# Optimization experiments

Measured on AMD Instinct MI355X. Metric: run time of the kernel, lower is better.

The kernel has to match this reference:

```python
import jax, jax.numpy as jnp
import numpy as np

INPUT_DIM, HIDDEN_DIM, OUTPUT_DIM = 64, 256, 32
BATCH, SEQ = 256, 1024
# AutoNCP(256, 32, sparsity_level=0.5): motor=32, command=max(int(0.4*224),1)=89, inter=135
LAYER_HID = [135, 89, 32]
LAYER_IN = [INPUT_DIM, 135, 89]


def setup_inputs() -> dict:
    key = jax.random.key(0)
    ks = iter(jax.random.split(key, 64))
    d = {}
    d["x"] = jax.random.normal(next(ks), (BATCH, SEQ, INPUT_DIM), dtype=jnp.float32)
    for l, (fin, hid) in enumerate(zip(LAYER_IN, LAYER_HID)):
        sp = jax.random.bernoulli(next(ks), 0.5, (hid, fin))
        d[f"mask{l}"] = jnp.concatenate([sp, jnp.ones((hid, hid), dtype=bool)], axis=1)
        scale = 1.0 / np.sqrt(fin + hid)
        for name in ("W1", "W2", "Wa", "Wb"):
            d[f"{name}_{l}"] = jax.random.normal(next(ks), (hid, fin + hid), dtype=jnp.float32) * scale
        for name in ("b1", "b2", "ba", "bb"):
            d[f"{name}_{l}"] = jnp.zeros((hid,), dtype=jnp.float32)
    d["fc_W"] = jax.random.normal(next(ks), (HIDDEN_DIM, HIDDEN_DIM), dtype=jnp.float32) * (1.0 / np.sqrt(HIDDEN_DIM))
    d["fc_b"] = jnp.zeros((HIDDEN_DIM,), dtype=jnp.float32)
    return d


def _cfc_cell(inp, h, mask, W1, b1, W2, b2, Wa, ba, Wb, bb):
    # ncps CfCCell, mode='default', no backbone, ts = 1.0
    x = jnp.concatenate([inp, h], axis=1)
    m = mask.astype(W1.dtype)
    ff1 = jnp.tanh(x @ (W1 * m).T + b1)
    ff2 = jnp.tanh(x @ (W2 * m).T + b2)
    t = jax.nn.sigmoid(x @ Wa.T + ba + x @ Wb.T + bb)  # sigmoid(t_a*ts + t_b), ts=1
    return ff1 * (1.0 - t) + t * ff2


def _forward(x, masks, layer_params, fc_W, fc_b):
    B = x.shape[0]
    init = tuple(jnp.zeros((B, h), dtype=x.dtype) for h in LAYER_HID)

    def step(carry, xt):
        hs = list(carry)
        inp = xt
        for l in range(3):  # inter -> command -> motor (WiredCfCCell)
            hs[l] = _cfc_cell(inp, hs[l], masks[l], *layer_params[l])
            inp = hs[l]
        return tuple(hs), None

    carry, _ = jax.lax.scan(step, init, jnp.swapaxes(x, 0, 1))  # scan over time [T,B,D]
    hn = jnp.concatenate(carry, axis=1)  # [B, HIDDEN_DIM] full state
    return hn @ fc_W.T + fc_b


def reference(x, mask0, mask1, mask2,
              W1_0, b1_0, W2_0, b2_0, Wa_0, ba_0, Wb_0, bb_0,
              W1_1, b1_1, W2_1, b2_1, Wa_1, ba_1, Wb_1, bb_1,
              W1_2, b1_2, W2_2, b2_2, Wa_2, ba_2, Wb_2, bb_2,
              fc_W, fc_b):
    masks = (mask0, mask1, mask2)
    lp = ((W1_0, b1_0, W2_0, b2_0, Wa_0, ba_0, Wb_0, bb_0),
          (W1_1, b1_1, W2_1, b2_1, Wa_1, ba_1, Wb_1, bb_1),
          (W1_2, b1_2, W2_2, b2_2, Wa_2, ba_2, Wb_2, bb_2))
    return _forward(x, masks, lp, fc_W, fc_b)
```

## Files before the change

### kernel.cpp

```cpp
#include <hip/hip_runtime.h>


typedef _Float16 half2v __attribute__((ext_vector_type(2)));
typedef _Float16 half8v __attribute__((ext_vector_type(8)));

#define NBLK   256
#define NTHR   512
#define TSTEPS 1024
#define KPAD   224
#define KHALF  112
#define NKB    14

struct Ptrs {
    const float* x;
    const unsigned int* msk[3];
    const float* W1[3];
    const float* W2[3];
    const float* Wa[3];
    const float* Wb[3];
    const float* b1[3];
    const float* b2[3];
    const float* ba[3];
    const float* bb[3];
    const float* fcW;
    const float* fcb;
};

__device__ __forceinline__ float fexp2(float x) {
#if __has_builtin(__builtin_amdgcn_exp2f)
    return __builtin_amdgcn_exp2f(x);
#else
    return exp2f(x);
#endif
}
__device__ __forceinline__ float frcp(float x) {
#if __has_builtin(__builtin_amdgcn_rcpf)
    return __builtin_amdgcn_rcpf(x);
#else
    return 1.0f / x;
#endif
}
__device__ __forceinline__ float fsig(float x) {
    return frcp(1.0f + fexp2(-1.442695041f * x));
}
__device__ __forceinline__ float ftanh(float x) {
    return 2.0f * frcp(1.0f + fexp2(-2.885390082f * x)) - 1.0f;
}

#if __has_builtin(__builtin_amdgcn_fdot2)
#define FD(a, b, c) __builtin_amdgcn_fdot2((a), (b), (c), false)
#else
__device__ __forceinline__ float fd_fallback(half2v a, half2v b, float c) {
    return c + (float)a[0] * (float)b[0] + (float)a[1] * (float)b[1];
}
#define FD(a, b, c) fd_fallback((a), (b), (c))
#endif

__global__ __launch_bounds__(NTHR)
__attribute__((amdgpu_waves_per_eu(2, 2)))
void cfc_kernel(Ptrs P, float* __restrict__ out) {
    __shared__ __align__(16) _Float16 xc[2][3][KPAD];
    __shared__ __align__(16) float hn[256];

    const int tid  = threadIdx.x;
    const int b    = blockIdx.x;
    const int pair = tid >> 1;
    const int half = tid & 1;

    int L, n;
    if (pair < 135)      { L = 0; n = pair; }
    else if (pair < 224) { L = 1; n = pair - 135; }
    else                 { L = 2; n = pair - 224; }
    const int K    = (L == 0) ? 199 : ((L == 1) ? 224 : 121);
    const int HOFF = (L == 0) ? 0   : ((L == 1) ? 135 : 224);

    {
        int* z = (int*)&xc[0][0][0];
        for (int i = tid; i < 2 * 3 * KPAD / 2; i += NTHR) z[i] = 0;
    }
    __syncthreads();

    const int xlane = tid - 448;
    float xpend = 0.0f;
    if (xlane >= 0) {
        xc[0][0][xlane] = (_Float16)P.x[((size_t)b * TSTEPS + 0) * 64 + xlane];
        xpend           = P.x[((size_t)b * TSTEPS + 1) * 64 + xlane];
    }

    const float* W1p        = P.W1[L];
    const float* W2p        = P.W2[L];
    const float* Wap        = P.Wa[L];
    const float* Wbp        = P.Wb[L];
    const unsigned int* mkp = P.msk[L];
    const int nK   = n * K;
    const int koff = half * KHALF;

    half2v wr1[KHALF / 2], wr2[KHALF / 2], wra[KHALF / 2];
#pragma unroll
    for (int i = 0; i < KHALF / 2; ++i) {
        const int k0 = koff + 2 * i, k1 = koff + 2 * i + 1;
        float u0 = 0.f, u1 = 0.f, v0 = 0.f, v1 = 0.f, a0 = 0.f, a1 = 0.f;
        if (k0 < K) {
            const int idx = nK + k0;
            const float mm = (mkp[idx] != 0u) ? 1.0f : 0.0f;
            u0 = W1p[idx] * mm;
            v0 = W2p[idx] * mm;
            a0 = Wap[idx] + Wbp[idx];
        }
        if (k1 < K) {
            const int idx = nK + k1;
            const float mm = (mkp[idx] != 0u) ? 1.0f : 0.0f;
            u1 = W1p[idx] * mm;
            v1 = W2p[idx] * mm;
            a1 = Wap[idx] + Wbp[idx];
        }
        wr1[i] = half2v{(_Float16)u0, (_Float16)u1};
        wr2[i] = half2v{(_Float16)v0, (_Float16)v1};
        wra[i] = half2v{(_Float16)a0, (_Float16)a1};
    }
    const float bv1 = P.b1[L][n];
    const float bv2 = P.b2[L][n];
    const float bva = P.ba[L][n] + P.bb[L][n];
    __syncthreads();

    for (int tick = 0; tick < TSTEPS + 2; ++tick) {
        if (xlane >= 0) {
            if (tick + 1 < TSTEPS)
                xc[(tick + 1) & 1][0][xlane] = (_Float16)xpend;
            if (tick + 2 < TSTEPS)
                xpend = P.x[((size_t)b * TSTEPS + (tick + 2)) * 64 + xlane];
        }

        const int s = tick - L;
        if (s >= 0 && s < TSTEPS) {
            const _Float16* src = &xc[s & 1][L][koff];
            float ac00 = 0.f, ac01 = 0.f, ac10 = 0.f, ac11 = 0.f, ac20 = 0.f, ac21 = 0.f;
#pragma unroll
            for (int kb = 0; kb < NKB; ++kb) {
                const half8v xv = *(const half8v*)(src + kb * 8);
                const half2v x0 = {xv[0], xv[1]};
                const half2v x1 = {xv[2], xv[3]};
                const half2v x2 = {xv[4], xv[5]};
                const half2v x3 = {xv[6], xv[7]};
                const int k4 = kb * 4;
                ac00 = FD(x0, wr1[k4 + 0], ac00);
                ac10 = FD(x0, wr2[k4 + 0], ac10);
                ac20 = FD(x0, wra[k4 + 0], ac20);
                ac01 = FD(x1, wr1[k4 + 1], ac01);
                ac11 = FD(x1, wr2[k4 + 1], ac11);
                ac21 = FD(x1, wra[k4 + 1], ac21);
                ac00 = FD(x2, wr1[k4 + 2], ac00);
                ac10 = FD(x2, wr2[k4 + 2], ac10);
                ac20 = FD(x2, wra[k4 + 2], ac20);
                ac01 = FD(x3, wr1[k4 + 3], ac01);
                ac11 = FD(x3, wr2[k4 + 3], ac11);
                ac21 = FD(x3, wra[k4 + 3], ac21);
            }
            float s1 = ac00 + ac01;
            float s2 = ac10 + ac11;
            float sa = ac20 + ac21;
            s1 += __shfl_xor(s1, 1, 64);
            s2 += __shfl_xor(s2, 1, 64);
            sa += __shfl_xor(sa, 1, 64);
            const float f1 = ftanh(s1 + bv1);
            const float f2 = ftanh(s2 + bv2);
            const float tg = fsig(sa + bva);
            const float h  = f1 + tg * (f2 - f1);
            const _Float16 hv = (_Float16)h;

            const int pA = s & 1;
            const int pB = (s + 1) & 1;
            if (half == 0) {
                if (L == 0)      xc[pA][1][n] = hv;
                else if (L == 1) xc[pA][2][n] = hv;
                if (s == TSTEPS - 1) hn[HOFF + n] = h;
            } else {
                if (L == 0)      xc[pB][0][64 + n]  = hv;
                else if (L == 1) xc[pB][1][135 + n] = hv;
                else             xc[pB][2][89 + n]  = hv;
            }
        }
        __syncthreads();
    }

    {
        const int o = pair;
        const float4* wr = (const float4*)(P.fcW + (size_t)o * 256 + half * 128);
        const float4* hr = (const float4*)(hn + half * 128);
        float acc = half ? 0.0f : P.fcb[o];
#pragma unroll 8
        for (int d = 0; d < 32; ++d) {
            const float4 a = hr[d];
            const float4 w = wr[d];
            acc += a.x * w.x + a.y * w.y + a.z * w.z + a.w * w.w;
        }
        acc += __shfl_xor(acc, 1, 64);
        if (half == 0) out[(size_t)b * 256 + o] = acc;
    }
}

extern "C" void kernel_launch(void* const* d_in, const int* in_sizes, int n_in,
                              void* d_out, int out_size, void* d_ws, size_t ws_size,
                              hipStream_t stream) {
    (void)in_sizes; (void)n_in; (void)out_size; (void)d_ws; (void)ws_size;
    Ptrs P;
    P.x = (const float*)d_in[0];
    for (int l = 0; l < 3; ++l) {
        const int base = 1 + l * 9;
        P.msk[l] = (const unsigned int*)d_in[base + 0];
        P.W1[l]  = (const float*)d_in[base + 1];
        P.W2[l]  = (const float*)d_in[base + 2];
        P.Wa[l]  = (const float*)d_in[base + 3];
        P.Wb[l]  = (const float*)d_in[base + 4];
        P.b1[l]  = (const float*)d_in[base + 5];
        P.b2[l]  = (const float*)d_in[base + 6];
        P.ba[l]  = (const float*)d_in[base + 7];
        P.bb[l]  = (const float*)d_in[base + 8];
    }
    P.fcW = (const float*)d_in[28];
    P.fcb = (const float*)d_in[29];

    hipLaunchKernelGGL(cfc_kernel, dim3(NBLK), dim3(NTHR), 0, stream,
                       P, (float*)d_out);
}
```

Before: 1.472 ms.

## Precompute layer-0 input projections per time window and split thread roles by layer

Measured after the change: 1.636 ms. 1.11x slower.

```diff
diff --git a/kernel.cpp b/kernel.cpp
--- a/kernel.cpp
+++ b/kernel.cpp
@@ -8,8 +8,7 @@
 #define NTHR   512
 #define TSTEPS 1024
 #define KPAD   224
-#define KHALF  112
-#define NKB    14
+#define WIN    64
 
 struct Ptrs {
     const float* x;
@@ -56,23 +55,64 @@
 #define FD(a, b, c) fd_fallback((a), (b), (c))
 #endif
 
+__device__ __forceinline__ half2v h2(_Float16 a, _Float16 b) { return half2v{a, b}; }
+
+__device__ __forceinline__ float psum(float x) { return x + __shfl_xor(x, 1, 64); }
+
+#define DOJOB(jj_) { \
+    const int jm = (jj_) >> 7, jn = (jj_) & 127; \
+    const float* Wp = (jm == 0) ? P.W1[0] : (jm == 1) ? P.W2[0] : P.Wa[0]; \
+    const float* Wq = P.Wb[0]; \
+    const unsigned int* mk0 = P.msk[0]; \
+    const int base = jn * 199; \
+    half2v wrow[32]; \
+    _Pragma("unroll") \
+    for (int i2 = 0; i2 < 32; ++i2) { \
+        const int k = 2 * i2; \
+        float v0 = Wp[base + k], v1 = Wp[base + k + 1]; \
+        if (jm == 2) { v0 += Wq[base + k]; v1 += Wq[base + k + 1]; } \
+        else { \
+            v0 = (mk0[base + k] != 0u) ? v0 : 0.0f; \
+            v1 = (mk0[base + k + 1] != 0u) ? v1 : 0.0f; \
+        } \
+        wrow[i2] = h2((_Float16)v0, (_Float16)v1); \
+    } \
+    for (int ti = 0; ti < WIN; ++ti) { \
+        float acc = 0.0f; \
+        _Pragma("unroll") \
+        for (int q = 0; q < 8; ++q) { \
+            const half8v xq = *(const half8v*)&xwin[ti][8 * q]; \
+            acc = FD(h2(xq[0], xq[1]), wrow[4 * q + 0], acc); \
+            acc = FD(h2(xq[2], xq[3]), wrow[4 * q + 1], acc); \
+            acc = FD(h2(xq[4], xq[5]), wrow[4 * q + 2], acc); \
+            acc = FD(h2(xq[6], xq[7]), wrow[4 * q + 3], acc); \
+        } \
+        U[jm][ti][jn] = (_Float16)acc; \
+    } \
+}
+
+#define WINDOW_BLOCK(STAGE_, JOBS_) \
+    if ((tick & (WIN - 1)) == 0 && tick < TSTEPS) { \
+        __syncthreads(); \
+        STAGE_ \
+        __syncthreads(); \
+        JOBS_ \
+        __syncthreads(); \
+    }
+
 __global__ __launch_bounds__(NTHR)
-__attribute__((amdgpu_waves_per_eu(2, 2)))
 void cfc_kernel(Ptrs P, float* __restrict__ out) {
     __shared__ __align__(16) _Float16 xc[2][3][KPAD];
-    __shared__ __align__(16) float hn[256];
+    __shared__ __align__(16) float    hn[256];
+    __shared__ __align__(16) _Float16 U[3][WIN][128];
+    __shared__ __align__(16) _Float16 wa0[128][152];
+    __shared__ __align__(16) _Float16 wa1[128][232];
+    __shared__ __align__(16) _Float16 xwin[WIN][64];
 
     const int tid  = threadIdx.x;
     const int b    = blockIdx.x;
-    const int pair = tid >> 1;
+    const int unit = tid >> 1;
     const int half = tid & 1;
-
-    int L, n;
-    if (pair < 135)      { L = 0; n = pair; }
-    else if (pair < 224) { L = 1; n = pair - 135; }
-    else                 { L = 2; n = pair - 224; }
-    const int K    = (L == 0) ? 199 : ((L == 1) ? 224 : 121);
-    const int HOFF = (L == 0) ? 0   : ((L == 1) ? 135 : 224);
 
     {
         int* z = (int*)&xc[0][0][0];
@@ -80,111 +120,255 @@
     }
     __syncthreads();
 
-    const int xlane = tid - 448;
-    float xpend = 0.0f;
-    if (xlane >= 0) {
-        xc[0][0][xlane] = (_Float16)P.x[((size_t)b * TSTEPS + 0) * 64 + xlane];
-        xpend           = P.x[((size_t)b * TSTEPS + 1) * 64 + xlane];
-    }
-
-    const float* W1p        = P.W1[L];
-    const float* W2p        = P.W2[L];
-    const float* Wap        = P.Wa[L];
-    const float* Wbp        = P.Wb[L];
-    const unsigned int* mkp = P.msk[L];
-    const int nK   = n * K;
-    const int koff = half * KHALF;
-
-    half2v wr1[KHALF / 2], wr2[KHALF / 2], wra[KHALF / 2];
-#pragma unroll
-    for (int i = 0; i < KHALF / 2; ++i) {
-        const int k0 = koff + 2 * i, k1 = koff + 2 * i + 1;
-        float u0 = 0.f, u1 = 0.f, v0 = 0.f, v1 = 0.f, a0 = 0.f, a1 = 0.f;
-        if (k0 < K) {
-            const int idx = nK + k0;
-            const float mm = (mkp[idx] != 0u) ? 1.0f : 0.0f;
-            u0 = W1p[idx] * mm;
-            v0 = W2p[idx] * mm;
-            a0 = Wap[idx] + Wbp[idx];
-        }
-        if (k1 < K) {
-            const int idx = nK + k1;
-            const float mm = (mkp[idx] != 0u) ? 1.0f : 0.0f;
-            u1 = W1p[idx] * mm;
-            v1 = W2p[idx] * mm;
-            a1 = Wap[idx] + Wbp[idx];
-        }
-        wr1[i] = half2v{(_Float16)u0, (_Float16)u1};
-        wr2[i] = half2v{(_Float16)v0, (_Float16)v1};
-        wra[i] = half2v{(_Float16)a0, (_Float16)a1};
-    }
-    const float bv1 = P.b1[L][n];
-    const float bv2 = P.b2[L][n];
-    const float bva = P.ba[L][n] + P.bb[L][n];
-    __syncthreads();
-
-    for (int tick = 0; tick < TSTEPS + 2; ++tick) {
-        if (xlane >= 0) {
+    const size_t rb = (size_t)b * TSTEPS;
+
+    if (tid < 256) {
+        const int n = unit;
+        const float* W1p = P.W1[0];
+        const float* W2p = P.W2[0];
+        const float* Wap = P.Wa[0];
+        const float* Wbp = P.Wb[0];
+        const int nK = n * 199;
+
+        half2v w1h[36], w2h[36];
+#pragma unroll
+        for (int i = 0; i < 36; ++i) {
+            const int c = 64 + 72 * half + 2 * i;
+            float u0 = (c < 199)     ? W1p[nK + c]     : 0.0f;
+            float u1 = (c + 1 < 199) ? W1p[nK + c + 1] : 0.0f;
+            float v0 = (c < 199)     ? W2p[nK + c]     : 0.0f;
+            float v1 = (c + 1 < 199) ? W2p[nK + c + 1] : 0.0f;
+            w1h[i] = h2((_Float16)u0, (_Float16)u1);
+            w2h[i] = h2((_Float16)v0, (_Float16)v1);
+            float a0 = (c < 199)     ? Wap[nK + c] + Wbp[nK + c]         : 0.0f;
+            float a1 = (c + 1 < 199) ? Wap[nK + c + 1] + Wbp[nK + c + 1] : 0.0f;
+            *(half2v*)&wa0[n][72 * half + 2 * i] = h2((_Float16)a0, (_Float16)a1);
+        }
+        const float bv1 = P.b1[0][n];
+        const float bv2 = P.b2[0][n];
+        const float bva = P.ba[0][n] + P.bb[0][n];
+        __syncthreads();
+
+        for (int tick = 0; tick < TSTEPS + 2; ++tick) {
+            WINDOW_BLOCK(
+                if (tid < 64) {
+                    for (int ti = 0; ti < WIN; ++ti)
+                        xwin[ti][tid] = (_Float16)P.x[(rb + tick + ti) * 64 + tid];
+                },
+                { DOJOB(tid); if (tid < 64) { DOJOB(320 + tid); } }
+            )
+            const int s = tick;
+            if (s < TSTEPS) {
+                const _Float16* srcp = &xc[s & 1][0][64 + 72 * half];
+                const _Float16* wvp  = &wa0[n][72 * half];
+                float a0 = 0.f, a1 = 0.f, b0 = 0.f, b1 = 0.f, c0 = 0.f, c1 = 0.f;
+#pragma unroll
+                for (int kb = 0; kb < 9; ++kb) {
+                    const half8v xv = *(const half8v*)(srcp + kb * 8);
+                    const half8v wv = *(const half8v*)(wvp + kb * 8);
+                    const half2v x0 = h2(xv[0], xv[1]), x1 = h2(xv[2], xv[3]);
+                    const half2v x2 = h2(xv[4], xv[5]), x3 = h2(xv[6], xv[7]);
+                    a0 = FD(x0, w1h[kb * 4 + 0], a0); b0 = FD(x0, w2h[kb * 4 + 0], b0);
+                    c0 = FD(x0, h2(wv[0], wv[1]), c0);
+                    a1 = FD(x1, w1h[kb * 4 + 1], a1); b1 = FD(x1, w2h[kb * 4 + 1], b1);
+                    c1 = FD(x1, h2(wv[2], wv[3]), c1);
+                    a0 = FD(x2, w1h[kb * 4 + 2], a0); b0 = FD(x2, w2h[kb * 4 + 2], b0);
+                    c0 = FD(x2, h2(wv[4], wv[5]), c0);
+                    a1 = FD(x3, w1h[kb * 4 + 3], a1); b1 = FD(x3, w2h[kb * 4 + 3], b1);
+                    c1 = FD(x3, h2(wv[6], wv[7]), c1);
+                }
+                const int tw = s & (WIN - 1);
+                const float u1 = (float)U[0][tw][n];
+                const float u2 = (float)U[1][tw][n];
+                const float ua = (float)U[2][tw][n];
+                const float s1 = psum(a0 + a1) + u1 + bv1;
+                const float s2 = psum(b0 + b1) + u2 + bv2;
+                const float sa = psum(c0 + c1) + ua + bva;
+                const float f1 = ftanh(s1);
+                const float f2 = ftanh(s2);
+                const float tg = fsig(sa);
+                const float h  = f1 + tg * (f2 - f1);
+                const _Float16 hv = (_Float16)h;
+                const int pA = s & 1, pB = (s + 1) & 1;
+                if (half == 0) {
+                    xc[pA][1][n] = hv;
+                    if (s == TSTEPS - 1) hn[n] = h;
+                } else {
+                    xc[pB][0][64 + n] = hv;
+                }
+            }
+            __syncthreads();
+        }
+    } else if (tid < 448) {
+        int L, n;
+        if (unit < 135) { L = 0; n = unit; } else { L = 1; n = unit - 135; }
+        const int K    = (L == 0) ? 199 : 224;
+        const int HOFF = (L == 0) ? 0 : 135;
+        const float* W1p = P.W1[L];
+        const float* W2p = P.W2[L];
+        const float* Wap = P.Wa[L];
+        const float* Wbp = P.Wb[L];
+        const unsigned int* mkp = P.msk[L];
+        const int nK   = n * K;
+        const int koff = 112 * half;
+        const int u128 = unit - 128;
+
+        half2v wr1[56], wr2[56];
+#pragma unroll
+        for (int i = 0; i < 56; ++i) {
+            const int k0 = koff + 2 * i, k1 = k0 + 1;
+            float u0 = 0.f, u1 = 0.f, v0 = 0.f, v1 = 0.f, a0 = 0.f, a1 = 0.f;
+            if (k0 < K) {
+                const int idx = nK + k0;
+                const float mm = (mkp[idx] != 0u) ? 1.0f : 0.0f;
+                u0 = W1p[idx] * mm; v0 = W2p[idx] * mm;
+                a0 = Wap[idx] + Wbp[idx];
+            }
+            if (k1 < K) {
+                const int idx = nK + k1;
+                const float mm = (mkp[idx] != 0u) ? 1.0f : 0.0f;
+                u1 = W1p[idx] * mm; v1 = W2p[idx] * mm;
+                a1 = Wap[idx] + Wbp[idx];
+            }
+            wr1[i] = h2((_Float16)u0, (_Float16)u1);
+            wr2[i] = h2((_Float16)v0, (_Float16)v1);
+            *(half2v*)&wa1[u128][k0] = h2((_Float16)a0, (_Float16)a1);
+        }
+        const float bv1 = P.b1[L][n];
+        const float bv2 = P.b2[L][n];
+        const float bva = P.ba[L][n] + P.bb[L][n];
+        __syncthreads();
+
+        for (int tick = 0; tick < TSTEPS + 2; ++tick) {
+            WINDOW_BLOCK(;, ;)
+            const int s = tick - L;
+            if (s >= 0 && s < TSTEPS) {
+                const _Float16* srcp = &xc[s & 1][L][koff];
+                const _Float16* wvp  = &wa1[u128][koff];
+                float a0 = 0.f, a1 = 0.f, b0 = 0.f, b1 = 0.f, c0 = 0.f, c1 = 0.f;
+#pragma unroll
+                for (int kb = 0; kb < 14; ++kb) {
+                    const half8v xv = *(const half8v*)(srcp + kb * 8);
+                    const half8v wv = *(const half8v*)(wvp + kb * 8);
+                    const half2v x0 = h2(xv[0], xv[1]), x1 = h2(xv[2], xv[3]);
+                    const half2v x2 = h2(xv[4], xv[5]), x3 = h2(xv[6], xv[7]);
+                    a0 = FD(x0, wr1[kb * 4 + 0], a0); b0 = FD(x0, wr2[kb * 4 + 0], b0);
+                    c0 = FD(x0, h2(wv[0], wv[1]), c0);
+                    a1 = FD(x1, wr1[kb * 4 + 1], a1); b1 = FD(x1, wr2[kb * 4 + 1], b1);
+                    c1 = FD(x1, h2(wv[2], wv[3]), c1);
+                    a0 = FD(x2, wr1[kb * 4 + 2], a0); b0 = FD(x2, wr2[kb * 4 + 2], b0);
+                    c0 = FD(x2, h2(wv[4], wv[5]), c0);
+                    a1 = FD(x3, wr1[kb * 4 + 3], a1); b1 = FD(x3, wr2[kb * 4 + 3], b1);
+                    c1 = FD(x3, h2(wv[6], wv[7]), c1);
+                }
+                const float s1 = psum(a0 + a1) + bv1;
+                const float s2 = psum(b0 + b1) + bv2;
+                const float sa = psum(c0 + c1) + bva;
+                const float f1 = ftanh(s1);
+                const float f2 = ftanh(s2);
+                const float tg = fsig(sa);
+                const float h  = f1 + tg * (f2 - f1);
+                const _Float16 hv = (_Float16)h;
+                const int pA = s & 1, pB = (s + 1) & 1;
+                if (half == 0) {
+                    if (L == 0) xc[pA][1][n] = hv; else xc[pA][2][n] = hv;
+                    if (s == TSTEPS - 1) hn[HOFF + n] = h;
+                } else {
+                    if (L == 0) xc[pB][0][64 + n] = hv; else xc[pB][1][135 + n] = hv;
+                }
+            }
+            __syncthreads();
+        }
+    } else {
+        const int n = unit - 224;
+        const float* W1p = P.W1[2];
+        const float* W2p = P.W2[2];
+        const float* Wap = P.Wa[2];
+        const float* Wbp = P.Wb[2];
+        const unsigned int* mkp = P.msk[2];
+        const int nK   = n * 121;
+        const int koff = 64 * half;
+        const int u128 = unit - 128;
+
+        half2v w1q[32], w2q[32];
+#pragma unroll
+        for (int i = 0; i < 32; ++i) {
+            const int k0 = koff + 2 * i, k1 = k0 + 1;
+            float u0 = 0.f, u1 = 0.f, v0 = 0.f, v1 = 0.f, a0 = 0.f, a1 = 0.f;
+            if (k0 < 121) {
+                const int idx = nK + k0;
+                const float mm = (mkp[idx] != 0u) ? 1.0f : 0.0f;
+                u0 = W1p[idx] * mm; v0 = W2p[idx] * mm;
+                a0 = Wap[idx] + Wbp[idx];
+            }
+            if (k1 < 121) {
+                const int idx = nK + k1;
+                const float mm = (mkp[idx] != 0u) ? 1.0f : 0.0f;
+                u1 = W1p[idx] * mm; v1 = W2p[idx] * mm;
+                a1 = Wap[idx] + Wbp[idx];
+            }
+            w1q[i] = h2((_Float16)u0, (_Float16)u1);
+            w2q[i] = h2((_Float16)v0, (_Float16)v1);
+            *(half2v*)&wa1[u128][k0] = h2((_Float16)a0, (_Float16)a1);
+        }
+        const float bv1 = P.b1[2][n];
+        const float bv2 = P.b2[2][n];
+        const float bva = P.ba[2][n] + P.bb[2][n];
+
+        const int xlane = tid - 448;
+        float xpend = 0.0f;
+        xc[0][0][xlane] = (_Float16)P.x[(rb + 0) * 64 + xlane];
+        xpend           = P.x[(rb + 1) * 64 + xlane];
+        __syncthreads();
+
+        for (int tick = 0; tick < TSTEPS + 2; ++tick) {
+            WINDOW_BLOCK(;, DOJOB(tid - 192);)
             if (tick + 1 < TSTEPS)
                 xc[(tick + 1) & 1][0][xlane] = (_Float16)xpend;
             if (tick + 2 < TSTEPS)
-                xpend = P.x[((size_t)b * TSTEPS + (tick + 2)) * 64 + xlane];
-        }
-
-        const int s = tick - L;
-        if (s >= 0 && s < TSTEPS) {
-            const _Float16* src = &xc[s & 1][L][koff];
-            float ac00 = 0.f, ac01 = 0.f, ac10 = 0.f, ac11 = 0.f, ac20 = 0.f, ac21 = 0.f;
-#pragma unroll
-            for (int kb = 0; kb < NKB; ++kb) {
-                const half8v xv = *(const half8v*)(src + kb * 8);
-                const half2v x0 = {xv[0], xv[1]};
-                const half2v x1 = {xv[2], xv[3]};
-                const half2v x2 = {xv[4], xv[5]};
-                const half2v x3 = {xv[6], xv[7]};
-                const int k4 = kb * 4;
-                ac00 = FD(x0, wr1[k4 + 0], ac00);
-                ac10 = FD(x0, wr2[k4 + 0], ac10);
-                ac20 = FD(x0, wra[k4 + 0], ac20);
-                ac01 = FD(x1, wr1[k4 + 1], ac01);
-                ac11 = FD(x1, wr2[k4 + 1], ac11);
-                ac21 = FD(x1, wra[k4 + 1], ac21);
-                ac00 = FD(x2, wr1[k4 + 2], ac00);
-                ac10 = FD(x2, wr2[k4 + 2], ac10);
-                ac20 = FD(x2, wra[k4 + 2], ac20);
-                ac01 = FD(x3, wr1[k4 + 3], ac01);
-                ac11 = FD(x3, wr2[k4 + 3], ac11);
-                ac21 = FD(x3, wra[k4 + 3], ac21);
-            }
-            float s1 = ac00 + ac01;
-            float s2 = ac10 + ac11;
-            float sa = ac20 + ac21;
-            s1 += __shfl_xor(s1, 1, 64);
-            s2 += __shfl_xor(s2, 1, 64);
-            sa += __shfl_xor(sa, 1, 64);
-            const float f1 = ftanh(s1 + bv1);
-            const float f2 = ftanh(s2 + bv2);
-            const float tg = fsig(sa + bva);
-            const float h  = f1 + tg * (f2 - f1);
-            const _Float16 hv = (_Float16)h;
-
-            const int pA = s & 1;
-            const int pB = (s + 1) & 1;
-            if (half == 0) {
-                if (L == 0)      xc[pA][1][n] = hv;
-                else if (L == 1) xc[pA][2][n] = hv;
-                if (s == TSTEPS - 1) hn[HOFF + n] = h;
-            } else {
-                if (L == 0)      xc[pB][0][64 + n]  = hv;
-                else if (L == 1) xc[pB][1][135 + n] = hv;
-                else             xc[pB][2][89 + n]  = hv;
-            }
-        }
-        __syncthreads();
+                xpend = P.x[(rb + (tick + 2)) * 64 + xlane];
+
+            const int s = tick - 2;
+            if (s >= 0 && s < TSTEPS) {
+                const _Float16* srcp = &xc[s & 1][2][koff];
+                const _Float16* wvp  = &wa1[u128][koff];
+                float a0 = 0.f, a1 = 0.f, b0 = 0.f, b1 = 0.f, c0 = 0.f, c1 = 0.f;
+#pragma unroll
+                for (int kb = 0; kb < 8; ++kb) {
+                    const half8v xv = *(const half8v*)(srcp + kb * 8);
+                    const half8v wv = *(const half8v*)(wvp + kb * 8);
+                    const half2v x0 = h2(xv[0], xv[1]), x1 = h2(xv[2], xv[3]);
+                    const half2v x2 = h2(xv[4], xv[5]), x3 = h2(xv[6], xv[7]);
+                    a0 = FD(x0, w1q[kb * 4 + 0], a0); b0 = FD(x0, w2q[kb * 4 + 0], b0);
+                    c0 = FD(x0, h2(wv[0], wv[1]), c0);
+                    a1 = FD(x1, w1q[kb * 4 + 1], a1); b1 = FD(x1, w2q[kb * 4 + 1], b1);
+                    c1 = FD(x1, h2(wv[2], wv[3]), c1);
+                    a0 = FD(x2, w1q[kb * 4 + 2], a0); b0 = FD(x2, w2q[kb * 4 + 2], b0);
+                    c0 = FD(x2, h2(wv[4], wv[5]), c0);
+                    a1 = FD(x3, w1q[kb * 4 + 3], a1); b1 = FD(x3, w2q[kb * 4 + 3], b1);
+                    c1 = FD(x3, h2(wv[6], wv[7]), c1);
+                }
+                const float s1 = psum(a0 + a1) + bv1;
+                const float s2 = psum(b0 + b1) + bv2;
+                const float sa = psum(c0 + c1) + bva;
+                const float f1 = ftanh(s1);
+                const float f2 = ftanh(s2);
+                const float tg = fsig(sa);
+                const float h  = f1 + tg * (f2 - f1);
+                const _Float16 hv = (_Float16)h;
+                const int pB = (s + 1) & 1;
+                if (half == 0) {
+                    if (s == TSTEPS - 1) hn[224 + n] = h;
+                } else {
+                    xc[pB][2][89 + n] = hv;
+                }
+            }
+            __syncthreads();
+        }
     }
 
     {
-        const int o = pair;
+        const int o = unit;
         const float4* wr = (const float4*)(P.fcW + (size_t)o * 256 + half * 128);
         const float4* hr = (const float4*)(hn + half * 128);
         float acc = half ? 0.0f : P.fcb[o];
@@ -194,7 +378,7 @@
             const float4 w = wr[d];
             acc += a.x * w.x + a.y * w.y + a.z * w.z + a.w * w.w;
         }
-        acc += __shfl_xor(acc, 1, 64);
+        acc = psum(acc);
         if (half == 0) out[(size_t)b * 256 + o] = acc;
     }
 }
```
